# Optimization experiments

Hardware: AMD Instinct MI355X
Metric: run time of the kernel (lower is better)

Reference implementation:

```python
import jax, jax.numpy as jnp
import numpy as np

N = 50000
E = 600000
IN_C = 128
OUT_C = 64
HID = 2 * OUT_C  # 128


def setup_inputs() -> dict:
    key = jax.random.key(0)
    ks = jax.random.split(key, 8)
    x = jax.random.normal(ks[0], (N, IN_C), dtype=jnp.float32)
    edge_index = jax.random.randint(ks[1], (2, E), 0, N, dtype=jnp.int64)
    # Glorot-style init for GCN weights, zero bias (PyG default)
    def glorot(k, fan_in, fan_out):
        s = jnp.sqrt(6.0 / (fan_in + fan_out)).astype(jnp.float32)
        return jax.random.uniform(k, (fan_in, fan_out), jnp.float32, -s, s)
    return {
        "x": x,
        "edge_index": edge_index,
        "W1": glorot(ks[2], IN_C, HID),
        "b1": jnp.zeros((HID,), jnp.float32),
        "W_mu": glorot(ks[3], HID, OUT_C),
        "b_mu": jnp.zeros((OUT_C,), jnp.float32),
        "W_ls": glorot(ks[4], HID, OUT_C),
        "b_ls": jnp.zeros((OUT_C,), jnp.float32),
    }


def _gcn_norm(edge_index, num_nodes):
    # Add self-loops, compute symmetric normalization (cached=True in original
    # means this is computed once and reused by all three convs -- same math).
    loop = jnp.arange(num_nodes, dtype=edge_index.dtype)
    row = jnp.concatenate([edge_index[0], loop])  # source
    col = jnp.concatenate([edge_index[1], loop])  # target
    deg = jax.ops.segment_sum(jnp.ones_like(col, dtype=jnp.float32), col,
                              num_segments=num_nodes)
    dis = jnp.where(deg > 0, jax.lax.rsqrt(deg), 0.0)  # deg^{-1/2}, inf->0
    norm = dis[row] * dis[col]  # [E+N]
    return row, col, norm


def _gcn_conv(x, W, b, row, col, norm, num_nodes):
    h = x @ W                                  # dense transform [N, out]
    msg = h[row] * norm[:, None]               # gather + scale [E+N, out]
    out = jax.ops.segment_sum(msg, col, num_segments=num_nodes)
    return out + b


def reference(x, edge_index, W1, b1, W_mu, b_mu, W_ls, b_ls):
    num_nodes = x.shape[0]
    row, col, norm = _gcn_norm(edge_index, num_nodes)
    # eval mode: F.dropout is identity when not training
    h = jax.nn.relu(_gcn_conv(x, W1, b1, row, col, norm, num_nodes))
    mu = _gcn_conv(h, W_mu, b_mu, row, col, norm, num_nodes)
    logstd = _gcn_conv(h, W_ls, b_ls, row, col, norm, num_nodes)
    return mu, logstd
```

## Files before the change

### kernel.cpp

```cpp
#include <hip/hip_runtime.h>
#include <hip/hip_fp16.h>


#define N_NODES 50000
#define N_EDGES 600000
#define MU_SIZE (N_NODES * 64)
#define WT_S 136
#define CAP 64

typedef _Float16 half8 __attribute__((ext_vector_type(8)));
typedef _Float16 half4 __attribute__((ext_vector_type(4)));
typedef float floatx4 __attribute__((ext_vector_type(4)));

union H8 { __half2 h2[4]; float4 f4; };

__global__ __launch_bounds__(256) void prep_kernel(const float* __restrict__ W1,
                                                   const float* __restrict__ Wmu,
                                                   const float* __restrict__ Wls,
                                                   _Float16* __restrict__ W1T,
                                                   _Float16* __restrict__ W2T,
                                                   int* __restrict__ fillcnt,
                                                   __half* __restrict__ zrowA,
                                                   __half* __restrict__ zrowB) {
  int idx = blockIdx.x * 256 + threadIdx.x;
  for (int z = idx; z < N_NODES; z += 32768) fillcnt[z] = 0;
  if (idx < 128) {
    zrowA[idx] = __float2half(0.f);
    zrowB[idx] = __float2half(0.f);
  }
  int e = idx & 16383;
  int n = e >> 7, k = e & 127;
  if (idx < 16384) {
    W1T[e] = (_Float16)W1[k * 128 + n];
  } else {
    float w = (n < 64) ? Wmu[k * 64 + n] : Wls[k * 64 + (n - 64)];
    W2T[e] = (_Float16)w;
  }
}

__global__ __launch_bounds__(256) void fill_kernel(const int* __restrict__ row,
                                                   const int* __restrict__ col,
                                                   int* __restrict__ fillcnt,
                                                   int* __restrict__ srcidx, int e) {
  int i = blockIdx.x * 256 + threadIdx.x;
  if (i < e) {
    int c = col[i];
    int pos = atomicAdd(&fillcnt[c], 1);
    if (pos < CAP) srcidx[(c << 6) + pos] = row[i];
  }
}

template <bool SPLIT>
__global__ __launch_bounds__(256) void gemm_mfma_kernel(const float* __restrict__ X,
                                                        const _Float16* __restrict__ Xh,
                                                        const _Float16* __restrict__ WT,
                                                        const int* __restrict__ fillcnt,
                                                        const float* __restrict__ ba,
                                                        const float* __restrict__ bb,
                                                        _Float16* __restrict__ Yh,
                                                        float* __restrict__ Yf) {
  __shared__ _Float16 WL[128 * WT_S];

  int t = threadIdx.x;
  for (int idx = t; idx < 128 * 16; idx += 256) {
    int n = idx >> 4, kk = (idx & 15) * 8;
    *(half8*)&WL[n * WT_S + kk] = *(const half8*)&WT[n * 128 + kk];
  }
  __syncthreads();

  int wid = t >> 6, lane = t & 63;
  int q = lane >> 4, m = lane & 15;
  const int ngroups = (N_NODES + 63) / 64;

  for (int g64 = blockIdx.x; g64 < ngroups; g64 += gridDim.x) {
    int node = g64 * 64 + wid * 16 + m;
    size_t nr = (size_t)min(node, N_NODES - 1);
    bool valid = node < N_NODES;

    half8 xfrag[4];
    if (!SPLIT) {
#pragma unroll
      for (int c = 0; c < 4; ++c) {
        const float* ap = &X[nr * 128 + 32 * c + 8 * q];
        float4 a0 = *(const float4*)ap;
        float4 a1 = *(const float4*)(ap + 4);
        half8 af = {(_Float16)a0.x, (_Float16)a0.y, (_Float16)a0.z, (_Float16)a0.w,
                    (_Float16)a1.x, (_Float16)a1.y, (_Float16)a1.z, (_Float16)a1.w};
        xfrag[c] = af;
      }
    } else {
#pragma unroll
      for (int c = 0; c < 4; ++c) {
        xfrag[c] = *(const half8*)&Xh[nr * 128 + 32 * c + 8 * q];
      }
    }
    float dnode = SPLIT ? 0.f : rsqrtf((float)(fillcnt[nr] + 1));

#pragma unroll
    for (int f = 0; f < 8; ++f) {
      floatx4 acc = {0.f, 0.f, 0.f, 0.f};
#pragma unroll
      for (int c = 0; c < 4; ++c) {
        half8 wfrag = *(const half8*)&WL[(16 * f + m) * WT_S + 32 * c + 8 * q];
        acc = __builtin_amdgcn_mfma_f32_16x16x32_f16(wfrag, xfrag[c], acc, 0, 0, 0);
      }
      int fbase = 16 * f + 4 * q;
      if (!SPLIT) {
        if (valid) {
          half4 o = {(_Float16)(acc[0] * dnode), (_Float16)(acc[1] * dnode),
                     (_Float16)(acc[2] * dnode), (_Float16)(acc[3] * dnode)};
          *(half4*)&Yh[(size_t)node * 128 + fbase] = o;
        }
      } else {
        float4 bias = (f < 4) ? *(const float4*)&ba[fbase]
                              : *(const float4*)&bb[fbase - 64];
        float4 o = make_float4(acc[0] + bias.x, acc[1] + bias.y, acc[2] + bias.z,
                               acc[3] + bias.w);
        if (valid) {
          if (f < 4)
            *(float4*)&Yf[(size_t)node * 64 + fbase] = o;
          else
            *(float4*)&Yf[MU_SIZE + (size_t)node * 64 + (fbase - 64)] = o;
        }
      }
    }
  }
}

template <bool BIAS_RELU>
__global__ __launch_bounds__(256) void aggregate_kernel(const __half* __restrict__ Hs,
                                                        const int* __restrict__ fillcnt,
                                                        const int* __restrict__ srcidx,
                                                        const float* __restrict__ bias,
                                                        __half* __restrict__ outH, int n) {
  int wid = threadIdx.x >> 6, lane = threadIdx.x & 63;
  int q = lane >> 4, ql = lane & 15;
  int i = blockIdx.x * 16 + wid * 4 + q;
  if (i >= n) return;
  int deg = fillcnt[i];
  float di = rsqrtf((float)(deg + 1));
  int cnt = min(deg, CAP);
  int base = i << 6;
  float4 selfv = ((const float4*)(Hs + (size_t)i * 128))[ql];
  float acc[8] = {0.f, 0.f, 0.f, 0.f, 0.f, 0.f, 0.f, 0.f};
  for (int k = 0; k < cnt; k += 8) {
    int r0 = srcidx[base + k + 0], r1 = srcidx[base + k + 1];
    int r2 = srcidx[base + k + 2], r3 = srcidx[base + k + 3];
    int r4 = srcidx[base + k + 4], r5 = srcidx[base + k + 5];
    int r6 = srcidx[base + k + 6], r7 = srcidx[base + k + 7];
    r0 = (k + 0 < cnt) ? r0 : N_NODES;
    r1 = (k + 1 < cnt) ? r1 : N_NODES;
    r2 = (k + 2 < cnt) ? r2 : N_NODES;
    r3 = (k + 3 < cnt) ? r3 : N_NODES;
    r4 = (k + 4 < cnt) ? r4 : N_NODES;
    r5 = (k + 5 < cnt) ? r5 : N_NODES;
    r6 = (k + 6 < cnt) ? r6 : N_NODES;
    r7 = (k + 7 < cnt) ? r7 : N_NODES;
    float4 v0 = ((const float4*)(Hs + (size_t)r0 * 128))[ql];
    float4 v1 = ((const float4*)(Hs + (size_t)r1 * 128))[ql];
    float4 v2 = ((const float4*)(Hs + (size_t)r2 * 128))[ql];
    float4 v3 = ((const float4*)(Hs + (size_t)r3 * 128))[ql];
    float4 v4 = ((const float4*)(Hs + (size_t)r4 * 128))[ql];
    float4 v5 = ((const float4*)(Hs + (size_t)r5 * 128))[ql];
    float4 v6 = ((const float4*)(Hs + (size_t)r6 * 128))[ql];
    float4 v7 = ((const float4*)(Hs + (size_t)r7 * 128))[ql];
    const __half2* a0 = (const __half2*)&v0;
    const __half2* a1 = (const __half2*)&v1;
    const __half2* a2 = (const __half2*)&v2;
    const __half2* a3 = (const __half2*)&v3;
    const __half2* a4 = (const __half2*)&v4;
    const __half2* a5 = (const __half2*)&v5;
    const __half2* a6 = (const __half2*)&v6;
    const __half2* a7 = (const __half2*)&v7;
#pragma unroll
    for (int j = 0; j < 4; ++j) {
      float2 f0 = __half22float2(a0[j]);
      float2 f1 = __half22float2(a1[j]);
      float2 f2 = __half22float2(a2[j]);
      float2 f3 = __half22float2(a3[j]);
      float2 f4 = __half22float2(a4[j]);
      float2 f5 = __half22float2(a5[j]);
      float2 f6 = __half22float2(a6[j]);
      float2 f7 = __half22float2(a7[j]);
      acc[2 * j] += ((f0.x + f1.x) + (f2.x + f3.x)) + ((f4.x + f5.x) + (f6.x + f7.x));
      acc[2 * j + 1] += ((f0.y + f1.y) + (f2.y + f3.y)) + ((f4.y + f5.y) + (f6.y + f7.y));
    }
  }
  const __half2* sh = (const __half2*)&selfv;
  float2 f0 = __half22float2(sh[0]);
  float2 f1 = __half22float2(sh[1]);
  float2 f2 = __half22float2(sh[2]);
  float2 f3 = __half22float2(sh[3]);
  float s0 = di * (acc[0] + f0.x), s1 = di * (acc[1] + f0.y);
  float s2 = di * (acc[2] + f1.x), s3 = di * (acc[3] + f1.y);
  float s4 = di * (acc[4] + f2.x), s5 = di * (acc[5] + f2.y);
  float s6 = di * (acc[6] + f3.x), s7 = di * (acc[7] + f3.y);
  H8 u;
  if (BIAS_RELU) {
    float4 b0 = ((const float4*)bias)[2 * ql];
    float4 b1 = ((const float4*)bias)[2 * ql + 1];
    u.h2[0] = __float22half2_rn(
        make_float2(di * fmaxf(s0 + b0.x, 0.f), di * fmaxf(s1 + b0.y, 0.f)));
    u.h2[1] = __float22half2_rn(
        make_float2(di * fmaxf(s2 + b0.z, 0.f), di * fmaxf(s3 + b0.w, 0.f)));
    u.h2[2] = __float22half2_rn(
        make_float2(di * fmaxf(s4 + b1.x, 0.f), di * fmaxf(s5 + b1.y, 0.f)));
    u.h2[3] = __float22half2_rn(
        make_float2(di * fmaxf(s6 + b1.z, 0.f), di * fmaxf(s7 + b1.w, 0.f)));
  } else {
    u.h2[0] = __float22half2_rn(make_float2(s0, s1));
    u.h2[1] = __float22half2_rn(make_float2(s2, s3));
    u.h2[2] = __float22half2_rn(make_float2(s4, s5));
    u.h2[3] = __float22half2_rn(make_float2(s6, s7));
  }
  ((float4*)(outH + (size_t)i * 128))[ql] = u.f4;
}

extern "C" void kernel_launch(void* const* d_in, const int* in_sizes, int n_in,
                              void* d_out, int out_size, void* d_ws, size_t ws_size,
                              hipStream_t stream) {
  const float* x = (const float*)d_in[0];
  const int* ei = (const int*)d_in[1];
  const float* W1 = (const float*)d_in[2];
  const float* b1 = (const float*)d_in[3];
  const float* Wmu = (const float*)d_in[4];
  const float* bmu = (const float*)d_in[5];
  const float* Wls = (const float*)d_in[6];
  const float* bls = (const float*)d_in[7];
  float* out = (float*)d_out;

  const int* row = ei;
  const int* col = ei + N_EDGES;

  __half* bufAh = (__half*)d_ws;
  __half* bufBh = bufAh + 6400128;
  __half* bufCh = bufBh + 6400128;
  int* fillcnt = (int*)(bufCh + 6400000);
  _Float16* W1T = (_Float16*)(fillcnt + N_NODES);
  _Float16* W2T = W1T + 16384;
  int* srcidx = (int*)(W2T + 16384);

  prep_kernel<<<128, 256, 0, stream>>>(W1, Wmu, Wls, W1T, W2T, fillcnt,
                                       bufAh + (size_t)N_NODES * 128,
                                       bufBh + (size_t)N_NODES * 128);

  int eb = (N_EDGES + 255) / 256;
  fill_kernel<<<eb, 256, 0, stream>>>(row, col, fillcnt, srcidx, N_EDGES);

  gemm_mfma_kernel<false><<<512, 256, 0, stream>>>(x, nullptr, W1T, fillcnt, nullptr,
                                                   nullptr, (_Float16*)bufAh, nullptr);
  int ab = (N_NODES + 15) / 16;
  aggregate_kernel<true><<<ab, 256, 0, stream>>>(bufAh, fillcnt, srcidx, b1,
                                                 bufBh, N_NODES);
  aggregate_kernel<false><<<ab, 256, 0, stream>>>(bufBh, fillcnt, srcidx,
                                                  nullptr, bufCh, N_NODES);
  gemm_mfma_kernel<true><<<512, 256, 0, stream>>>(nullptr, (const _Float16*)bufCh, W2T,
                                                  fillcnt, bmu, bls, nullptr, out);
}
```

Before: 187.2 us.

## Merge prep and CSR fill into cooperative kernel; store 16-bit neighbor indices

Merges the weight-transpose/zeroing kernel and the edge-bucketing fill kernel into one cooperative launch with a grid-wide sync, removing one kernel launch. Neighbor indices are stored as 16-bit values, halving the index traffic, and the aggregate loop now loads eight indices with one 128-bit vector load. Loop bounds use the wave-wide max count so the vector loads stay uniform. Risk: node ids up to 49999 fit in 16 bits only for this N, and a cooperative launch of 512 blocks must fit co-resident.

```diff
diff --git a/kernel.cpp b/kernel.cpp
--- a/kernel.cpp
+++ b/kernel.cpp
@@ -1,5 +1,8 @@
 #include <hip/hip_runtime.h>
 #include <hip/hip_fp16.h>
+#include <hip/hip_cooperative_groups.h>
+
+namespace cg = cooperative_groups;
 
 
 #define N_NODES 50000
@@ -14,39 +17,33 @@
 
 union H8 { __half2 h2[4]; float4 f4; };
 
-__global__ __launch_bounds__(256) void prep_kernel(const float* __restrict__ W1,
-                                                   const float* __restrict__ Wmu,
-                                                   const float* __restrict__ Wls,
-                                                   _Float16* __restrict__ W1T,
-                                                   _Float16* __restrict__ W2T,
-                                                   int* __restrict__ fillcnt,
-                                                   __half* __restrict__ zrowA,
-                                                   __half* __restrict__ zrowB) {
+__global__ __launch_bounds__(256) void setup_fill_kernel(
+    const float* __restrict__ W1, const float* __restrict__ Wmu,
+    const float* __restrict__ Wls, _Float16* __restrict__ W1T,
+    _Float16* __restrict__ W2T, int* __restrict__ fillcnt,
+    __half* __restrict__ zrowA, __half* __restrict__ zrowB,
+    const int* __restrict__ row, const int* __restrict__ col,
+    unsigned short* __restrict__ srcidx) {
   int idx = blockIdx.x * 256 + threadIdx.x;
-  for (int z = idx; z < N_NODES; z += 32768) fillcnt[z] = 0;
+  for (int z = idx; z < N_NODES; z += 131072) fillcnt[z] = 0;
   if (idx < 128) {
     zrowA[idx] = __float2half(0.f);
     zrowB[idx] = __float2half(0.f);
   }
-  int e = idx & 16383;
-  int n = e >> 7, k = e & 127;
   if (idx < 16384) {
-    W1T[e] = (_Float16)W1[k * 128 + n];
-  } else {
+    int n = idx >> 7, k = idx & 127;
+    W1T[idx] = (_Float16)W1[k * 128 + n];
+  } else if (idx < 32768) {
+    int e = idx - 16384;
+    int n = e >> 7, k = e & 127;
     float w = (n < 64) ? Wmu[k * 64 + n] : Wls[k * 64 + (n - 64)];
     W2T[e] = (_Float16)w;
   }
-}
-
-__global__ __launch_bounds__(256) void fill_kernel(const int* __restrict__ row,
-                                                   const int* __restrict__ col,
-                                                   int* __restrict__ fillcnt,
-                                                   int* __restrict__ srcidx, int e) {
-  int i = blockIdx.x * 256 + threadIdx.x;
-  if (i < e) {
+  cg::this_grid().sync();
+  for (int i = idx; i < N_EDGES; i += 131072) {
     int c = col[i];
     int pos = atomicAdd(&fillcnt[c], 1);
-    if (pos < CAP) srcidx[(c << 6) + pos] = row[i];
+    if (pos < CAP) srcidx[(c << 6) + pos] = (unsigned short)row[i];
   }
 }
 
@@ -128,11 +125,10 @@
 }
 
 template <bool BIAS_RELU>
-__global__ __launch_bounds__(256) void aggregate_kernel(const __half* __restrict__ Hs,
-                                                        const int* __restrict__ fillcnt,
-                                                        const int* __restrict__ srcidx,
-                                                        const float* __restrict__ bias,
-                                                        __half* __restrict__ outH, int n) {
+__global__ __launch_bounds__(256) void aggregate_kernel(
+    const __half* __restrict__ Hs, const int* __restrict__ fillcnt,
+    const unsigned short* __restrict__ srcidx, const float* __restrict__ bias,
+    __half* __restrict__ outH, int n) {
   int wid = threadIdx.x >> 6, lane = threadIdx.x & 63;
   int q = lane >> 4, ql = lane & 15;
   int i = blockIdx.x * 16 + wid * 4 + q;
@@ -140,14 +136,17 @@
   int deg = fillcnt[i];
   float di = rsqrtf((float)(deg + 1));
   int cnt = min(deg, CAP);
-  int base = i << 6;
+  int mc = max(cnt, __shfl_xor(cnt, 16));
+  mc = max(mc, __shfl_xor(mc, 32));
+  const unsigned short* sp = srcidx + ((size_t)i << 6);
   float4 selfv = ((const float4*)(Hs + (size_t)i * 128))[ql];
   float acc[8] = {0.f, 0.f, 0.f, 0.f, 0.f, 0.f, 0.f, 0.f};
-  for (int k = 0; k < cnt; k += 8) {
-    int r0 = srcidx[base + k + 0], r1 = srcidx[base + k + 1];
-    int r2 = srcidx[base + k + 2], r3 = srcidx[base + k + 3];
-    int r4 = srcidx[base + k + 4], r5 = srcidx[base + k + 5];
-    int r6 = srcidx[base + k + 6], r7 = srcidx[base + k + 7];
+  for (int k = 0; k < mc; k += 8) {
+    uint4 idv = *(const uint4*)(sp + k);
+    int r0 = (int)(idv.x & 0xffffu), r1 = (int)(idv.x >> 16);
+    int r2 = (int)(idv.y & 0xffffu), r3 = (int)(idv.y >> 16);
+    int r4 = (int)(idv.z & 0xffffu), r5 = (int)(idv.z >> 16);
+    int r6 = (int)(idv.w & 0xffffu), r7 = (int)(idv.w >> 16);
     r0 = (k + 0 < cnt) ? r0 : N_NODES;
     r1 = (k + 1 < cnt) ? r1 : N_NODES;
     r2 = (k + 2 < cnt) ? r2 : N_NODES;
@@ -238,14 +237,16 @@
   int* fillcnt = (int*)(bufCh + 6400000);
   _Float16* W1T = (_Float16*)(fillcnt + N_NODES);
   _Float16* W2T = W1T + 16384;
-  int* srcidx = (int*)(W2T + 16384);
-
-  prep_kernel<<<128, 256, 0, stream>>>(W1, Wmu, Wls, W1T, W2T, fillcnt,
-                                       bufAh + (size_t)N_NODES * 128,
-                                       bufBh + (size_t)N_NODES * 128);
-
-  int eb = (N_EDGES + 255) / 256;
-  fill_kernel<<<eb, 256, 0, stream>>>(row, col, fillcnt, srcidx, N_EDGES);
+  unsigned short* srcidx = (unsigned short*)(W2T + 16384);
+
+  __half* zrowA = bufAh + (size_t)N_NODES * 128;
+  __half* zrowB = bufBh + (size_t)N_NODES * 128;
+
+  void* cargs[] = {(void*)&W1,    (void*)&Wmu,   (void*)&Wls,  (void*)&W1T,
+                   (void*)&W2T,   (void*)&fillcnt, (void*)&zrowA, (void*)&zrowB,
+                   (void*)&row,   (void*)&col,   (void*)&srcidx};
+  hipLaunchCooperativeKernel((void*)setup_fill_kernel, dim3(512), dim3(256),
+                             cargs, 0, stream);
 
   gemm_mfma_kernel<false><<<512, 256, 0, stream>>>(x, nullptr, W1T, fillcnt, nullptr,
                                                    nullptr, (_Float16*)bufAh, nullptr);
```

Result: slower. 257.5 us (+37.5%).
